# Kernel tuning notes

Measured on AMD Instinct MI355X. Metric: run time of the kernel, lower is better.

## Reference

```python
import jax, jax.numpy as jnp
import numpy as np

B, T, D, F, E, K = 2, 2048, 1024, 4096, 8, 2

def setup_inputs() -> dict:
    key = jax.random.key(0)
    k0, k1, k2, k3 = jax.random.split(key, 4)
    return {
        "x": jax.random.normal(k0, (B, T, D), jnp.float32),
        "Wg": jax.random.normal(k1, (D, E), jnp.float32) * (D ** -0.5),
        "W1": jax.random.normal(k2, (E, D, F), jnp.float32) * (D ** -0.5),
        "b1": jnp.zeros((E, F), jnp.float32),
        "W2": jax.random.normal(k3, (E, F, D), jnp.float32) * (F ** -0.5),
        "b2": jnp.zeros((E, D), jnp.float32),
        "topk": K,
    }

def reference(x, Wg, W1, b1, W2, b2, topk):
    n_experts = Wg.shape[-1]
    # Gating logits [B, T, E]
    gating = jnp.einsum('btd,de->bte', x, Wg)
    _, idx = jax.lax.top_k(gating, topk)
    # 0/1 mask of selected experts per token [B, T, E]
    mask = jax.nn.one_hot(idx, n_experts, dtype=x.dtype).sum(axis=-2)
    # Source does `gating -= 1/mask - 1`: no-op where mask==1, -inf where mask==0
    gate = jax.nn.softmax(jnp.where(mask > 0, gating, -jnp.inf), axis=-1)
    # Dense masked per-expert compute, exactly as the source (expert(x * mask_e))
    xm = x[:, :, None, :] * mask[:, :, :, None]          # [B, T, E, D]
    h = jax.nn.gelu(jnp.einsum('bted,edf->btef', xm, W1) + b1)  # [B, T, E, F]
    out_e = jnp.einsum('btef,efd->bted', h, W2) + b2     # [B, T, E, D]
    # Gate and sum over experts
    return jnp.sum(out_e * gate[..., None], axis=-2)      # [B, T, D]
```

## Files before the change

kernel.cpp:

```cpp
#include <hip/hip_runtime.h>
#include <hip/hip_bf16.h>
#include <math.h>

#define NB 2
#define NT 2048
#define NTOK 4096
#define DD 1024
#define FF 4096
#define NE 8
#define KSEL 2
#define BM 128
#define BN 128
#define BK 64
#define ROWCAP 9216
#define ROWTILES 72
#define KP2 2

typedef __attribute__((ext_vector_type(8))) short short8_t;
typedef __attribute__((ext_vector_type(4))) float f32x4;

__device__ __forceinline__ unsigned short f2bf(float f){
  unsigned u = __float_as_uint(f);
  unsigned r = (u + 0x7fffu + ((u >> 16) & 1u)) >> 16;
  return (unsigned short)r;
}

__device__ __forceinline__ int xcd_swz(int lin, int nwg){
  int q = nwg >> 3, r = nwg & 7;
  int xcd = lin & 7, idx = lin >> 3;
  return (xcd < r ? xcd * (q + 1) : r * (q + 1) + (xcd - r) * q) + idx;
}

#define GLOAD_LDS(g, l) \
  __builtin_amdgcn_global_load_lds((const __attribute__((address_space(1))) void*)(g), \
                                   (__attribute__((address_space(3))) void*)(l), 16, 0, 0)


__global__ void k_prep(const float* __restrict__ x, const float* __restrict__ wg,
                       short* __restrict__ xb, int* __restrict__ topk_idx,
                       float* __restrict__ topk_gate, int* __restrict__ counts){
  int wid = threadIdx.x >> 6, lane = threadIdx.x & 63;
  int t = blockIdx.x * 4 + wid;
  const float* xr = x + (size_t)t * DD;
  short* xbr = xb + (size_t)t * DD;
  double acc[NE];
#pragma unroll
  for (int e = 0; e < NE; ++e) acc[e] = 0.0;
#pragma unroll
  for (int p = 0; p < 4; ++p){
    int d = p * 256 + lane * 4;
    float4 v = *(const float4*)(xr + d);
    short4 o;
    o.x = (short)f2bf(v.x); o.y = (short)f2bf(v.y);
    o.z = (short)f2bf(v.z); o.w = (short)f2bf(v.w);
    *(short4*)(xbr + d) = o;
    const float* w0 = wg + (size_t)d * NE;
    float vv[4] = {v.x, v.y, v.z, v.w};
#pragma unroll
    for (int j = 0; j < 4; ++j){
      double xv = (double)vv[j];
#pragma unroll
      for (int e = 0; e < NE; ++e) acc[e] += xv * (double)w0[j * NE + e];
    }
  }
#pragma unroll
  for (int e = 0; e < NE; ++e){
#pragma unroll
    for (int s = 32; s; s >>= 1) acc[e] += __shfl_xor(acc[e], s, 64);
  }
  if (lane == 0){
    int i0 = 0; double v0 = acc[0];
#pragma unroll
    for (int e = 1; e < NE; ++e) if (acc[e] > v0){ v0 = acc[e]; i0 = e; }
    int i1 = -1; double v1 = -1e300;
#pragma unroll
    for (int e = 0; e < NE; ++e) if (e != i0 && acc[e] > v1){ v1 = acc[e]; i1 = e; }
    double g0 = 1.0 / (1.0 + exp(v1 - v0));
    topk_idx[2 * t] = i0; topk_idx[2 * t + 1] = i1;
    topk_gate[2 * t] = (float)g0; topk_gate[2 * t + 1] = (float)(1.0 - g0);
    atomicAdd(&counts[i0], 1);
    atomicAdd(&counts[i1], 1);
  }
}


__global__ void k_transpose_all(const float* __restrict__ W1, const float* __restrict__ W2,
                                short* __restrict__ w1t, short* __restrict__ w2t){
  __shared__ short T[64][132];
  int id = blockIdx.x;
  bool isW2 = id >= 4096;
  int rem = id & 4095;
  int e = rem >> 9;
  int tr = rem & 511;
  int R, C, c0, r0;
  const float* in; short* out;
  if (!isW2){ R = DD; C = FF; c0 = (tr & 63) * 64; r0 = (tr >> 6) * 128;
              in = W1 + (size_t)e * R * C; out = w1t + (size_t)e * R * C; }
  else      { R = FF; C = DD; c0 = (tr & 15) * 64; r0 = (tr >> 4) * 128;
              in = W2 + (size_t)e * R * C; out = w2t + (size_t)e * R * C; }
  int t = threadIdx.x;
  int rr = t >> 4, c4 = (t & 15) * 4;
#pragma unroll
  for (int p = 0; p < 8; ++p){
    int row = p * 16 + rr;
    float4 v = *(const float4*)(in + (size_t)(r0 + row) * C + c0 + c4);
    T[c4 + 0][row] = (short)f2bf(v.x);
    T[c4 + 1][row] = (short)f2bf(v.y);
    T[c4 + 2][row] = (short)f2bf(v.z);
    T[c4 + 3][row] = (short)f2bf(v.w);
  }
  __syncthreads();
  int c8 = (t & 15) * 8;
#pragma unroll
  for (int q = 0; q < 4; ++q){
    int orow = q * 16 + rr;
    short4 lo = *(const short4*)&T[orow][c8];
    short4 hi = *(const short4*)&T[orow][c8 + 4];
    short8_t w;
    w[0] = lo.x; w[1] = lo.y; w[2] = lo.z; w[3] = lo.w;
    w[4] = hi.x; w[5] = hi.y; w[6] = hi.z; w[7] = hi.w;
    *(short8_t*)(out + (size_t)(c0 + orow) * R + r0 + c8) = w;
  }
}


__global__ void k_route_all(const int* __restrict__ counts, const int* __restrict__ topk_idx,
                            const float* __restrict__ topk_gate, int* __restrict__ poff_g,
                            int* __restrict__ row_token, float* __restrict__ row_gate,
                            int* __restrict__ slot_of){
  __shared__ int poff[NE + 1], cur[NE], rends[NE];
  if (threadIdx.x == 0){
    int off = 0;
    for (int e = 0; e < NE; ++e){
      poff[e] = off; cur[e] = off; rends[e] = off + counts[e];
      off += (counts[e] + BM - 1) & ~(BM - 1);
    }
    poff[NE] = off;
    for (int e = 0; e <= NE; ++e) poff_g[e] = poff[e];
  }
  __syncthreads();
  for (int t = threadIdx.x; t < NTOK; t += 256){
#pragma unroll
    for (int k = 0; k < KSEL; ++k){
      int e = topk_idx[2 * t + k];
      float g = topk_gate[2 * t + k];
      int slot = atomicAdd(&cur[e], 1);
      row_token[slot] = t;
      row_gate[slot] = g;
      slot_of[2 * t + k] = slot;
    }
  }
  __syncthreads();
#pragma unroll
  for (int e = 0; e < NE; ++e)
    for (int s = rends[e] + (int)threadIdx.x; s < poff[e + 1]; s += 256){
      row_token[s] = 0; row_gate[s] = 0.f;
    }
}


__launch_bounds__(256, 4)
__global__ void k_gemm1(const short* __restrict__ xb, const short* __restrict__ w1t,
                        const float* __restrict__ b1, short* __restrict__ h,
                        const int* __restrict__ row_token, const int* __restrict__ poff){
  __shared__ short As[BM * BK];
  __shared__ short Bs[BN * BK];
  int lin = blockIdx.x + ROWTILES * blockIdx.y;
  int wg = xcd_swz(lin, ROWTILES * (FF / BN));
  int bx = wg >> 5, by = wg & 31;
  int row0 = bx * BM;
  if (row0 >= poff[NE]) return;
  int e = 0;
  while (row0 >= poff[e + 1]) ++e;
  int n0 = by * BN;
  int tid = threadIdx.x;

  const short* asrc[4]; const short* bsrc[4];
#pragma unroll
  for (int p = 0; p < 4; ++p){
    int L = p * 256 + tid;
    int r = L >> 3, cs = L & 7;
    int cd = cs ^ (r & 7);
    int tok = row_token[row0 + r];
    asrc[p] = xb + (size_t)tok * DD + cd * 8;
    bsrc[p] = w1t + (size_t)e * FF * DD + (size_t)(n0 + r) * DD + cd * 8;
  }
  short* alds = As + tid * 8;
  short* blds = Bs + tid * 8;

  f32x4 acc[4][4];
#pragma unroll
  for (int i = 0; i < 4; ++i)
#pragma unroll
    for (int j = 0; j < 4; ++j) acc[i][j] = (f32x4){0.f, 0.f, 0.f, 0.f};

  int wid = tid >> 6, lane = tid & 63;
  int wr = wid >> 1, wc = wid & 1;
  int lrow = lane & 15, lk = lane >> 4;

  for (int k0 = 0; k0 < DD; k0 += BK){
#pragma unroll
    for (int p = 0; p < 4; ++p){
      GLOAD_LDS(asrc[p] + k0, alds + p * 2048);
      GLOAD_LDS(bsrc[p] + k0, blds + p * 2048);
    }
    __syncthreads();
#pragma unroll
    for (int kk = 0; kk < 2; ++kk){
      short8_t a[4], b[4];
      int c = kk * 4 + lk;
#pragma unroll
      for (int m = 0; m < 4; ++m){
        int r = wr * 64 + m * 16 + lrow;
        a[m] = *(const short8_t*)(As + r * BK + ((c ^ (r & 7)) * 8));
      }
#pragma unroll
      for (int n = 0; n < 4; ++n){
        int r = wc * 64 + n * 16 + lrow;
        b[n] = *(const short8_t*)(Bs + r * BK + ((c ^ (r & 7)) * 8));
      }
#pragma unroll
      for (int m = 0; m < 4; ++m)
#pragma unroll
        for (int n = 0; n < 4; ++n)
          acc[m][n] = __builtin_amdgcn_mfma_f32_16x16x32_bf16(a[m], b[n], acc[m][n], 0, 0, 0);
    }
    __syncthreads();
  }

  const float* b1e = b1 + (size_t)e * FF;
#pragma unroll
  for (int n = 0; n < 4; ++n){
    int col = n0 + wc * 64 + n * 16 + lrow;
    float bias = b1e[col];
#pragma unroll
    for (int m = 0; m < 4; ++m){
#pragma unroll
      for (int j = 0; j < 4; ++j){
        int row = row0 + wr * 64 + m * 16 + lk * 4 + j;
        float v = acc[m][n][j] + bias;
        float u = 0.7978845608028654f * (v + 0.044715f * v * v * v);
        float g = v / (1.0f + __expf(-2.0f * u));
        h[(size_t)row * FF + col] = (short)f2bf(g);
      }
    }
  }
}


__launch_bounds__(256, 4)
__global__ void k_gemm2(const short* __restrict__ h, const short* __restrict__ w2t,
                        const float* __restrict__ b2, float* __restrict__ ya,
                        float* __restrict__ yb, const int* __restrict__ poff){
  __shared__ short As[BM * BK];
  __shared__ short Bs[BN * BK];
  int lin = blockIdx.x + ROWTILES * (blockIdx.y + (DD / BN) * blockIdx.z);
  int wg = xcd_swz(lin, ROWTILES * (DD / BN) * KP2);
  int by = wg & 7, bx = (wg >> 3) % ROWTILES, kz = (wg >> 3) / ROWTILES;
  int row0 = bx * BM;
  if (row0 >= poff[NE]) return;
  int e = 0;
  while (row0 >= poff[e + 1]) ++e;
  int n0 = by * BN;
  int tid = threadIdx.x;

  const short* asrc[4]; const short* bsrc[4];
#pragma unroll
  for (int p = 0; p < 4; ++p){
    int L = p * 256 + tid;
    int r = L >> 3, cs = L & 7;
    int cd = cs ^ (r & 7);
    asrc[p] = h + (size_t)(row0 + r) * FF + cd * 8;
    bsrc[p] = w2t + (size_t)e * DD * FF + (size_t)(n0 + r) * FF + cd * 8;
  }
  short* alds = As + tid * 8;
  short* blds = Bs + tid * 8;

  f32x4 acc[4][4];
#pragma unroll
  for (int i = 0; i < 4; ++i)
#pragma unroll
    for (int j = 0; j < 4; ++j) acc[i][j] = (f32x4){0.f, 0.f, 0.f, 0.f};

  int wid = tid >> 6, lane = tid & 63;
  int wr = wid >> 1, wc = wid & 1;
  int lrow = lane & 15, lk = lane >> 4;

  int kbeg = kz * (FF / KP2), kend = kbeg + FF / KP2;
  for (int k0 = kbeg; k0 < kend; k0 += BK){
#pragma unroll
    for (int p = 0; p < 4; ++p){
      GLOAD_LDS(asrc[p] + k0, alds + p * 2048);
      GLOAD_LDS(bsrc[p] + k0, blds + p * 2048);
    }
    __syncthreads();
#pragma unroll
    for (int kk = 0; kk < 2; ++kk){
      short8_t a[4], b[4];
      int c = kk * 4 + lk;
#pragma unroll
      for (int m = 0; m < 4; ++m){
        int r = wr * 64 + m * 16 + lrow;
        a[m] = *(const short8_t*)(As + r * BK + ((c ^ (r & 7)) * 8));
      }
#pragma unroll
      for (int n = 0; n < 4; ++n){
        int r = wc * 64 + n * 16 + lrow;
        b[n] = *(const short8_t*)(Bs + r * BK + ((c ^ (r & 7)) * 8));
      }
#pragma unroll
      for (int m = 0; m < 4; ++m)
#pragma unroll
        for (int n = 0; n < 4; ++n)
          acc[m][n] = __builtin_amdgcn_mfma_f32_16x16x32_bf16(a[m], b[n], acc[m][n], 0, 0, 0);
    }
    __syncthreads();
  }

  float* y = (kz == 0) ? ya : yb;
  const float* b2e = b2 + (size_t)e * DD;
#pragma unroll
  for (int n = 0; n < 4; ++n){
    int col = n0 + wc * 64 + n * 16 + lrow;
    float bias = (kz == 0) ? b2e[col] : 0.0f;
#pragma unroll
    for (int m = 0; m < 4; ++m){
#pragma unroll
      for (int j = 0; j < 4; ++j){
        int row = row0 + wr * 64 + m * 16 + lk * 4 + j;
        y[(size_t)row * DD + col] = acc[m][n][j] + bias;
      }
    }
  }
}


__global__ void k_combine(const float* __restrict__ ya, const float* __restrict__ yb,
                          const int* __restrict__ slot_of, const float* __restrict__ topk_gate,
                          float* __restrict__ out){
  int i = blockIdx.x * 256 + threadIdx.x;
  int t = i >> 8;
  int c4 = (i & 255) * 4;
  int s0 = slot_of[2 * t], s1 = slot_of[2 * t + 1];
  float g0 = topk_gate[2 * t], g1 = topk_gate[2 * t + 1];
  float4 a0 = *(const float4*)(ya + (size_t)s0 * DD + c4);
  float4 b0 = *(const float4*)(yb + (size_t)s0 * DD + c4);
  float4 a1 = *(const float4*)(ya + (size_t)s1 * DD + c4);
  float4 b1 = *(const float4*)(yb + (size_t)s1 * DD + c4);
  float4 o;
  o.x = g0 * (a0.x + b0.x) + g1 * (a1.x + b1.x);
  o.y = g0 * (a0.y + b0.y) + g1 * (a1.y + b1.y);
  o.z = g0 * (a0.z + b0.z) + g1 * (a1.z + b1.z);
  o.w = g0 * (a0.w + b0.w) + g1 * (a1.w + b1.w);
  *(float4*)(out + (size_t)t * DD + c4) = o;
}


extern "C" void kernel_launch(void* const* d_in, const int* in_sizes, int n_in,
                              void* d_out, int out_size, void* d_ws, size_t ws_size,
                              hipStream_t stream){
  (void)in_sizes; (void)n_in; (void)out_size; (void)ws_size;
  const float* x  = (const float*)d_in[0];
  const float* Wg = (const float*)d_in[1];
  const float* W1 = (const float*)d_in[2];
  const float* b1 = (const float*)d_in[3];
  const float* W2 = (const float*)d_in[4];
  const float* b2 = (const float*)d_in[5];
  float* out = (float*)d_out;
  char* ws = (char*)d_ws;

  int*   counts    = (int*)(ws + 0);
  int*   poff      = (int*)(ws + 256);
  int*   topk_idx  = (int*)(ws + 1024);
  float* topk_gate = (float*)(ws + 33792);
  int*   row_token = (int*)(ws + 66560);
  float* row_gate  = (float*)(ws + 103424);
  int*   slot_of   = (int*)(ws + 140288);
  short* xb        = (short*)(ws + 173056);
  short* w1t       = (short*)(ws + 8561664);
  short* w2t       = (short*)(ws + 75670528);
  short* h         = (short*)(ws + 142779392);
  float* ya        = (float*)(ws + 173056);
  float* yb        = (float*)(ws + 37921792);

  hipMemsetAsync(counts, 0, 32, stream);

  k_prep<<<dim3(NTOK / 4), 256, 0, stream>>>(x, Wg, xb, topk_idx, topk_gate, counts);
  k_transpose_all<<<dim3(8192), 256, 0, stream>>>(W1, W2, w1t, w2t);
  k_route_all<<<dim3(1), 256, 0, stream>>>(counts, topk_idx, topk_gate, poff,
                                           row_token, row_gate, slot_of);
  k_gemm1<<<dim3(ROWTILES, FF / BN), 256, 0, stream>>>(xb, w1t, b1, h, row_token, poff);
  k_gemm2<<<dim3(ROWTILES, DD / BN, KP2), 256, 0, stream>>>(h, w2t, b2, ya, yb, poff);
  k_combine<<<dim3(NTOK * DD / 4 / 256), 256, 0, stream>>>(ya, yb, slot_of, topk_gate, out);
}
```

Before: 473.9 us.

## Rewrite expert GEMMs with 256x256 double-buffered tiles and atomic gated scatter

Both expert GEMMs move to 512-thread blocks computing 256x256 tiles. The K loop now double-buffers LDS and interleaves the next tile's async global-to-LDS loads with MFMA phases, using raw barriers and priority hints. The combine kernel and the split-K y buffers are replaced by per-element gated atomicAdd into a zeroed output, with split-K raised to 4. GEMM1's epilogue stages GELU results through LDS to make vector stores. The weight transposes are split so W2's transpose runs after GEMM1 and reuses the xb workspace. The change aims for more operand reuse and latency hiding, but the float atomics add contention and make summation order nondeterministic.

```diff
diff --git a/kernel.cpp b/kernel.cpp
--- a/kernel.cpp
+++ b/kernel.cpp
@@ -2,27 +2,22 @@
 #include <hip/hip_bf16.h>
 #include <math.h>
 
-#define NB 2
-#define NT 2048
 #define NTOK 4096
 #define DD 1024
 #define FF 4096
 #define NE 8
 #define KSEL 2
-#define BM 128
-#define BN 128
 #define BK 64
-#define ROWCAP 9216
-#define ROWTILES 72
-#define KP2 2
+#define PADR 256
+#define MT 40
+#define KP2 4
 
 typedef __attribute__((ext_vector_type(8))) short short8_t;
 typedef __attribute__((ext_vector_type(4))) float f32x4;
 
 __device__ __forceinline__ unsigned short f2bf(float f){
   unsigned u = __float_as_uint(f);
-  unsigned r = (u + 0x7fffu + ((u >> 16) & 1u)) >> 16;
-  return (unsigned short)r;
+  return (unsigned short)((u + 0x7fffu + ((u >> 16) & 1u)) >> 16);
 }
 
 __device__ __forceinline__ int xcd_swz(int lin, int nwg){
@@ -34,6 +29,11 @@
 #define GLOAD_LDS(g, l) \
   __builtin_amdgcn_global_load_lds((const __attribute__((address_space(1))) void*)(g), \
                                    (__attribute__((address_space(3))) void*)(l), 16, 0, 0)
+#define VMCNT0 asm volatile("s_waitcnt vmcnt(0)" ::: "memory")
+#define RAWBAR __builtin_amdgcn_s_barrier()
+#define SCHEDB __builtin_amdgcn_sched_barrier(0)
+#define PRIO1 __builtin_amdgcn_s_setprio(1)
+#define PRIO0 __builtin_amdgcn_s_setprio(0)
 
 
 __global__ void k_prep(const float* __restrict__ x, const float* __restrict__ wg,
@@ -84,20 +84,16 @@
 }
 
 
-__global__ void k_transpose_all(const float* __restrict__ W1, const float* __restrict__ W2,
-                                short* __restrict__ w1t, short* __restrict__ w2t){
+__global__ void k_transpose(const float* __restrict__ W, short* __restrict__ Wt, int isW2){
   __shared__ short T[64][132];
   int id = blockIdx.x;
-  bool isW2 = id >= 4096;
-  int rem = id & 4095;
-  int e = rem >> 9;
-  int tr = rem & 511;
+  int e = id >> 9;
+  int tr = id & 511;
   int R, C, c0, r0;
-  const float* in; short* out;
-  if (!isW2){ R = DD; C = FF; c0 = (tr & 63) * 64; r0 = (tr >> 6) * 128;
-              in = W1 + (size_t)e * R * C; out = w1t + (size_t)e * R * C; }
-  else      { R = FF; C = DD; c0 = (tr & 15) * 64; r0 = (tr >> 4) * 128;
-              in = W2 + (size_t)e * R * C; out = w2t + (size_t)e * R * C; }
+  if (!isW2){ R = DD; C = FF; c0 = (tr & 63) * 64; r0 = (tr >> 6) * 128; }
+  else      { R = FF; C = DD; c0 = (tr & 15) * 64; r0 = (tr >> 4) * 128; }
+  const float* in = W + (size_t)e * R * C;
+  short* out = Wt + (size_t)e * R * C;
   int t = threadIdx.x;
   int rr = t >> 4, c4 = (t & 15) * 4;
 #pragma unroll
@@ -126,14 +122,13 @@
 
 __global__ void k_route_all(const int* __restrict__ counts, const int* __restrict__ topk_idx,
                             const float* __restrict__ topk_gate, int* __restrict__ poff_g,
-                            int* __restrict__ row_token, float* __restrict__ row_gate,
-                            int* __restrict__ slot_of){
+                            int* __restrict__ row_token, float* __restrict__ row_gate){
   __shared__ int poff[NE + 1], cur[NE], rends[NE];
   if (threadIdx.x == 0){
     int off = 0;
     for (int e = 0; e < NE; ++e){
       poff[e] = off; cur[e] = off; rends[e] = off + counts[e];
-      off += (counts[e] + BM - 1) & ~(BM - 1);
+      off += (counts[e] + PADR - 1) & ~(PADR - 1);
     }
     poff[NE] = off;
     for (int e = 0; e <= NE; ++e) poff_g[e] = poff[e];
@@ -143,11 +138,9 @@
 #pragma unroll
     for (int k = 0; k < KSEL; ++k){
       int e = topk_idx[2 * t + k];
-      float g = topk_gate[2 * t + k];
       int slot = atomicAdd(&cur[e], 1);
       row_token[slot] = t;
-      row_gate[slot] = g;
-      slot_of[2 * t + k] = slot;
+      row_gate[slot] = topk_gate[2 * t + k];
     }
   }
   __syncthreads();
@@ -159,200 +152,272 @@
 }
 
 
-__launch_bounds__(256, 4)
+__launch_bounds__(512, 2)
 __global__ void k_gemm1(const short* __restrict__ xb, const short* __restrict__ w1t,
                         const float* __restrict__ b1, short* __restrict__ h,
                         const int* __restrict__ row_token, const int* __restrict__ poff){
-  __shared__ short As[BM * BK];
-  __shared__ short Bs[BN * BK];
-  int lin = blockIdx.x + ROWTILES * blockIdx.y;
-  int wg = xcd_swz(lin, ROWTILES * (FF / BN));
-  int bx = wg >> 5, by = wg & 31;
-  int row0 = bx * BM;
+  __shared__ short As[2][2][8192];
+  __shared__ short Bs[2][2][8192];
+  int lin = xcd_swz(blockIdx.x, MT * (FF / 256));
+  int chunk = lin / 80, idx = lin % 80;
+  int bx = chunk * 5 + idx % 5;
+  int by = idx / 5;
+  int row0 = bx * 256;
   if (row0 >= poff[NE]) return;
   int e = 0;
   while (row0 >= poff[e + 1]) ++e;
-  int n0 = by * BN;
+  int n0 = by * 256;
   int tid = threadIdx.x;
-
-  const short* asrc[4]; const short* bsrc[4];
-#pragma unroll
-  for (int p = 0; p < 4; ++p){
-    int L = p * 256 + tid;
-    int r = L >> 3, cs = L & 7;
-    int cd = cs ^ (r & 7);
-    int tok = row_token[row0 + r];
-    asrc[p] = xb + (size_t)tok * DD + cd * 8;
-    bsrc[p] = w1t + (size_t)e * FF * DD + (size_t)(n0 + r) * DD + cd * 8;
-  }
-  short* alds = As + tid * 8;
-  short* blds = Bs + tid * 8;
-
-  f32x4 acc[4][4];
-#pragma unroll
-  for (int i = 0; i < 4; ++i)
-#pragma unroll
-    for (int j = 0; j < 4; ++j) acc[i][j] = (f32x4){0.f, 0.f, 0.f, 0.f};
-
   int wid = tid >> 6, lane = tid & 63;
   int wr = wid >> 1, wc = wid & 1;
   int lrow = lane & 15, lk = lane >> 4;
 
-  for (int k0 = 0; k0 < DD; k0 += BK){
-#pragma unroll
-    for (int p = 0; p < 4; ++p){
-      GLOAD_LDS(asrc[p] + k0, alds + p * 2048);
-      GLOAD_LDS(bsrc[p] + k0, blds + p * 2048);
-    }
-    __syncthreads();
-#pragma unroll
-    for (int kk = 0; kk < 2; ++kk){
-      short8_t a[4], b[4];
-      int c = kk * 4 + lk;
-#pragma unroll
-      for (int m = 0; m < 4; ++m){
-        int r = wr * 64 + m * 16 + lrow;
-        a[m] = *(const short8_t*)(As + r * BK + ((c ^ (r & 7)) * 8));
-      }
-#pragma unroll
-      for (int n = 0; n < 4; ++n){
-        int r = wc * 64 + n * 16 + lrow;
-        b[n] = *(const short8_t*)(Bs + r * BK + ((c ^ (r & 7)) * 8));
-      }
-#pragma unroll
-      for (int m = 0; m < 4; ++m)
-#pragma unroll
-        for (int n = 0; n < 4; ++n)
-          acc[m][n] = __builtin_amdgcn_mfma_f32_16x16x32_bf16(a[m], b[n], acc[m][n], 0, 0, 0);
-    }
-    __syncthreads();
+  const short* a_src[2][2]; const short* b_src[2][2];
+  {
+    int r = tid >> 3, cd = (tid & 7) ^ (r & 7);
+    int r2 = (512 + tid) >> 3, cd2 = ((512 + tid) & 7) ^ (r2 & 7);
+#pragma unroll
+    for (int h2 = 0; h2 < 2; ++h2){
+      int tokA = row_token[row0 + h2 * 128 + r];
+      int tokB = row_token[row0 + h2 * 128 + r2];
+      a_src[h2][0] = xb + (size_t)tokA * DD + cd * 8;
+      a_src[h2][1] = xb + (size_t)tokB * DD + cd2 * 8;
+      b_src[h2][0] = w1t + (size_t)e * FF * DD + (size_t)(n0 + h2 * 128 + r) * DD + cd * 8;
+      b_src[h2][1] = w1t + (size_t)e * FF * DD + (size_t)(n0 + h2 * 128 + r2) * DD + cd2 * 8;
+    }
+  }
+
+  f32x4 acc[4][8];
+#pragma unroll
+  for (int i = 0; i < 4; ++i)
+#pragma unroll
+    for (int j = 0; j < 8; ++j) acc[i][j] = (f32x4){0.f, 0.f, 0.f, 0.f};
+
+  auto SA = [&](int nb, int k0){
+#pragma unroll
+    for (int h2 = 0; h2 < 2; ++h2){
+      GLOAD_LDS(a_src[h2][0] + k0, &As[nb][h2][0] + tid * 8);
+      GLOAD_LDS(a_src[h2][1] + k0, &As[nb][h2][0] + 4096 + tid * 8);
+    }
+  };
+  auto SB = [&](int nb, int k0){
+#pragma unroll
+    for (int h2 = 0; h2 < 2; ++h2){
+      GLOAD_LDS(b_src[h2][0] + k0, &Bs[nb][h2][0] + tid * 8);
+      GLOAD_LDS(b_src[h2][1] + k0, &Bs[nb][h2][0] + 4096 + tid * 8);
+    }
+  };
+  auto rdA = [&](const short* Ab, int kk, short8_t* av){
+#pragma unroll
+    for (int m = 0; m < 4; ++m){
+      int r = (wr & 1) * 64 + m * 16 + lrow;
+      av[m] = *(const short8_t*)(Ab + r * 64 + (((kk * 4 + lk) ^ (r & 7)) << 3));
+    }
+  };
+  auto rdB = [&](const short* Bb, int kk, short8_t* bv){
+#pragma unroll
+    for (int n = 0; n < 4; ++n){
+      int r = wc * 64 + n * 16 + lrow;
+      bv[n] = *(const short8_t*)(Bb + r * 64 + (((kk * 4 + lk) ^ (r & 7)) << 3));
+    }
+  };
+  auto MF = [&](int nh, short8_t* av, short8_t* bv){
+#pragma unroll
+    for (int m = 0; m < 4; ++m)
+#pragma unroll
+      for (int n = 0; n < 4; ++n)
+        acc[m][nh * 4 + n] = __builtin_amdgcn_mfma_f32_16x16x32_bf16(av[m], bv[n], acc[m][nh * 4 + n], 0, 0, 0);
+  };
+
+  SA(0, 0); SB(0, 0);
+  VMCNT0; RAWBAR; SCHEDB;
+
+  const int NKT = DD / BK;
+#pragma unroll 1
+  for (int g = 0; g < NKT; ++g){
+    int b = g & 1, nb = b ^ 1;
+    int k1 = (g + 1) * BK;
+    bool more = (g + 1 < NKT);
+    const short* Ab = &As[b][wr >> 1][0];
+    short8_t av[4], bv[4];
+    if (more) SA(nb, k1);
+    rdA(Ab, 0, av); rdB(&Bs[b][0][0], 0, bv);
+    RAWBAR; SCHEDB; PRIO1; MF(0, av, bv); PRIO0; RAWBAR; SCHEDB;
+    if (more) SB(nb, k1);
+    rdB(&Bs[b][1][0], 0, bv);
+    RAWBAR; SCHEDB; PRIO1; MF(1, av, bv); PRIO0; RAWBAR; SCHEDB;
+    rdA(Ab, 1, av); rdB(&Bs[b][0][0], 1, bv);
+    RAWBAR; SCHEDB; PRIO1; MF(0, av, bv); PRIO0; RAWBAR; SCHEDB;
+    rdB(&Bs[b][1][0], 1, bv);
+    RAWBAR; SCHEDB; PRIO1; MF(1, av, bv); PRIO0;
+    if (more) VMCNT0;
+    RAWBAR; SCHEDB;
   }
 
   const float* b1e = b1 + (size_t)e * FF;
-#pragma unroll
-  for (int n = 0; n < 4; ++n){
-    int col = n0 + wc * 64 + n * 16 + lrow;
-    float bias = b1e[col];
-#pragma unroll
-    for (int m = 0; m < 4; ++m){
-#pragma unroll
-      for (int j = 0; j < 4; ++j){
-        int row = row0 + wr * 64 + m * 16 + lk * 4 + j;
-        float v = acc[m][n][j] + bias;
-        float u = 0.7978845608028654f * (v + 0.044715f * v * v * v);
-        float g = v / (1.0f + __expf(-2.0f * u));
-        h[(size_t)row * FF + col] = (short)f2bf(g);
-      }
-    }
-  }
-}
-
-
-__launch_bounds__(256, 4)
-__global__ void k_gemm2(const short* __restrict__ h, const short* __restrict__ w2t,
-                        const float* __restrict__ b2, float* __restrict__ ya,
-                        float* __restrict__ yb, const int* __restrict__ poff){
-  __shared__ short As[BM * BK];
-  __shared__ short Bs[BN * BK];
-  int lin = blockIdx.x + ROWTILES * (blockIdx.y + (DD / BN) * blockIdx.z);
-  int wg = xcd_swz(lin, ROWTILES * (DD / BN) * KP2);
-  int by = wg & 7, bx = (wg >> 3) % ROWTILES, kz = (wg >> 3) / ROWTILES;
-  int row0 = bx * BM;
+  float bias8[8];
+#pragma unroll
+  for (int nh = 0; nh < 2; ++nh)
+#pragma unroll
+    for (int n = 0; n < 4; ++n)
+      bias8[nh * 4 + n] = b1e[n0 + nh * 128 + wc * 64 + n * 16 + lrow];
+  short* E = &As[0][0][0] + wid * 2048;
+#pragma unroll 1
+  for (int m = 0; m < 4; ++m){
+#pragma unroll
+    for (int nh = 0; nh < 2; ++nh)
+#pragma unroll
+      for (int n = 0; n < 4; ++n)
+#pragma unroll
+        for (int j = 0; j < 4; ++j){
+          float v = acc[m][nh * 4 + n][j] + bias8[nh * 4 + n];
+          float u = 0.7978845608028654f * (v + 0.044715f * v * v * v);
+          float gl = v / (1.0f + __expf(-2.0f * u));
+          E[(lk * 4 + j) * 128 + nh * 64 + n * 16 + lrow] = (short)f2bf(gl);
+        }
+#pragma unroll
+    for (int q = 0; q < 4; ++q){
+      int id = q * 64 + lane;
+      int r = id >> 4;
+      int c8 = id & 15;
+      short8_t w = *(const short8_t*)(E + r * 128 + c8 * 8);
+      int row = row0 + wr * 64 + m * 16 + r;
+      int col = n0 + (c8 >> 3) * 128 + wc * 64 + (c8 & 7) * 8;
+      *(short8_t*)(h + (size_t)row * FF + col) = w;
+    }
+  }
+}
+
+
+__launch_bounds__(512, 2)
+__global__ void k_gemm2(const short* __restrict__ hA, const short* __restrict__ w2t,
+                        const float* __restrict__ b2, float* __restrict__ out,
+                        const int* __restrict__ row_token, const float* __restrict__ row_gate,
+                        const int* __restrict__ poff){
+  __shared__ short As[2][2][8192];
+  __shared__ short Bs[2][2][8192];
+  int lin = xcd_swz(blockIdx.x, MT * (DD / 256) * KP2);
+  int chunk = lin / 80, idx = lin % 80;
+  int bx = chunk * 5 + idx % 5;
+  int by = (idx / 5) & 3;
+  int kz = idx / 20;
+  int row0 = bx * 256;
   if (row0 >= poff[NE]) return;
   int e = 0;
   while (row0 >= poff[e + 1]) ++e;
-  int n0 = by * BN;
+  int n0 = by * 256;
+  int kbeg = kz * (FF / KP2);
   int tid = threadIdx.x;
-
-  const short* asrc[4]; const short* bsrc[4];
-#pragma unroll
-  for (int p = 0; p < 4; ++p){
-    int L = p * 256 + tid;
-    int r = L >> 3, cs = L & 7;
-    int cd = cs ^ (r & 7);
-    asrc[p] = h + (size_t)(row0 + r) * FF + cd * 8;
-    bsrc[p] = w2t + (size_t)e * DD * FF + (size_t)(n0 + r) * FF + cd * 8;
-  }
-  short* alds = As + tid * 8;
-  short* blds = Bs + tid * 8;
-
-  f32x4 acc[4][4];
-#pragma unroll
-  for (int i = 0; i < 4; ++i)
-#pragma unroll
-    for (int j = 0; j < 4; ++j) acc[i][j] = (f32x4){0.f, 0.f, 0.f, 0.f};
-
   int wid = tid >> 6, lane = tid & 63;
   int wr = wid >> 1, wc = wid & 1;
   int lrow = lane & 15, lk = lane >> 4;
 
-  int kbeg = kz * (FF / KP2), kend = kbeg + FF / KP2;
-  for (int k0 = kbeg; k0 < kend; k0 += BK){
-#pragma unroll
-    for (int p = 0; p < 4; ++p){
-      GLOAD_LDS(asrc[p] + k0, alds + p * 2048);
-      GLOAD_LDS(bsrc[p] + k0, blds + p * 2048);
-    }
-    __syncthreads();
-#pragma unroll
-    for (int kk = 0; kk < 2; ++kk){
-      short8_t a[4], b[4];
-      int c = kk * 4 + lk;
-#pragma unroll
-      for (int m = 0; m < 4; ++m){
-        int r = wr * 64 + m * 16 + lrow;
-        a[m] = *(const short8_t*)(As + r * BK + ((c ^ (r & 7)) * 8));
+  const short* a_src[2][2]; const short* b_src[2][2];
+  {
+    int r = tid >> 3, cd = (tid & 7) ^ (r & 7);
+    int r2 = (512 + tid) >> 3, cd2 = ((512 + tid) & 7) ^ (r2 & 7);
+#pragma unroll
+    for (int h2 = 0; h2 < 2; ++h2){
+      a_src[h2][0] = hA + (size_t)(row0 + h2 * 128 + r) * FF + kbeg + cd * 8;
+      a_src[h2][1] = hA + (size_t)(row0 + h2 * 128 + r2) * FF + kbeg + cd2 * 8;
+      b_src[h2][0] = w2t + (size_t)e * DD * FF + (size_t)(n0 + h2 * 128 + r) * FF + kbeg + cd * 8;
+      b_src[h2][1] = w2t + (size_t)e * DD * FF + (size_t)(n0 + h2 * 128 + r2) * FF + kbeg + cd2 * 8;
+    }
+  }
+
+  f32x4 acc[4][8];
+#pragma unroll
+  for (int i = 0; i < 4; ++i)
+#pragma unroll
+    for (int j = 0; j < 8; ++j) acc[i][j] = (f32x4){0.f, 0.f, 0.f, 0.f};
+
+  auto SA = [&](int nb, int k0){
+#pragma unroll
+    for (int h2 = 0; h2 < 2; ++h2){
+      GLOAD_LDS(a_src[h2][0] + k0, &As[nb][h2][0] + tid * 8);
+      GLOAD_LDS(a_src[h2][1] + k0, &As[nb][h2][0] + 4096 + tid * 8);
+    }
+  };
+  auto SB = [&](int nb, int k0){
+#pragma unroll
+    for (int h2 = 0; h2 < 2; ++h2){
+      GLOAD_LDS(b_src[h2][0] + k0, &Bs[nb][h2][0] + tid * 8);
+      GLOAD_LDS(b_src[h2][1] + k0, &Bs[nb][h2][0] + 4096 + tid * 8);
+    }
+  };
+  auto rdA = [&](const short* Ab, int kk, short8_t* av){
+#pragma unroll
+    for (int m = 0; m < 4; ++m){
+      int r = (wr & 1) * 64 + m * 16 + lrow;
+      av[m] = *(const short8_t*)(Ab + r * 64 + (((kk * 4 + lk) ^ (r & 7)) << 3));
+    }
+  };
+  auto rdB = [&](const short* Bb, int kk, short8_t* bv){
+#pragma unroll
+    for (int n = 0; n < 4; ++n){
+      int r = wc * 64 + n * 16 + lrow;
+      bv[n] = *(const short8_t*)(Bb + r * 64 + (((kk * 4 + lk) ^ (r & 7)) << 3));
+    }
+  };
+  auto MF = [&](int nh, short8_t* av, short8_t* bv){
+#pragma unroll
+    for (int m = 0; m < 4; ++m)
+#pragma unroll
+      for (int n = 0; n < 4; ++n)
+        acc[m][nh * 4 + n] = __builtin_amdgcn_mfma_f32_16x16x32_bf16(av[m], bv[n], acc[m][nh * 4 + n], 0, 0, 0);
+  };
+
+  SA(0, 0); SB(0, 0);
+  VMCNT0; RAWBAR; SCHEDB;
+
+  const int NKT = (FF / KP2) / BK;
+#pragma unroll 1
+  for (int g = 0; g < NKT; ++g){
+    int b = g & 1, nb = b ^ 1;
+    int k1 = (g + 1) * BK;
+    bool more = (g + 1 < NKT);
+    const short* Ab = &As[b][wr >> 1][0];
+    short8_t av[4], bv[4];
+    if (more) SA(nb, k1);
+    rdA(Ab, 0, av); rdB(&Bs[b][0][0], 0, bv);
+    RAWBAR; SCHEDB; PRIO1; MF(0, av, bv); PRIO0; RAWBAR; SCHEDB;
+    if (more) SB(nb, k1);
+    rdB(&Bs[b][1][0], 0, bv);
+    RAWBAR; SCHEDB; PRIO1; MF(1, av, bv); PRIO0; RAWBAR; SCHEDB;
+    rdA(Ab, 1, av); rdB(&Bs[b][0][0], 1, bv);
+    RAWBAR; SCHEDB; PRIO1; MF(0, av, bv); PRIO0; RAWBAR; SCHEDB;
+    rdB(&Bs[b][1][0], 1, bv);
+    RAWBAR; SCHEDB; PRIO1; MF(1, av, bv); PRIO0;
+    if (more) VMCNT0;
+    RAWBAR; SCHEDB;
+  }
+
+  const float* b2e = b2 + (size_t)e * DD;
+  float bias8[8];
+#pragma unroll
+  for (int nh = 0; nh < 2; ++nh)
+#pragma unroll
+    for (int n = 0; n < 4; ++n)
+      bias8[nh * 4 + n] = (kz == 0) ? b2e[n0 + nh * 128 + wc * 64 + n * 16 + lrow] : 0.0f;
+#pragma unroll
+  for (int m = 0; m < 4; ++m){
+#pragma unroll
+    for (int j = 0; j < 4; ++j){
+      int row = row0 + wr * 64 + m * 16 + lk * 4 + j;
+      float gt = row_gate[row];
+      if (gt != 0.f){
+        int tok = row_token[row];
+        float* orow = out + (size_t)tok * DD;
+#pragma unroll
+        for (int nh = 0; nh < 2; ++nh)
+#pragma unroll
+          for (int n = 0; n < 4; ++n){
+            int col = n0 + nh * 128 + wc * 64 + n * 16 + lrow;
+            atomicAdd(&orow[col], gt * (acc[m][nh * 4 + n][j] + bias8[nh * 4 + n]));
+          }
       }
-#pragma unroll
-      for (int n = 0; n < 4; ++n){
-        int r = wc * 64 + n * 16 + lrow;
-        b[n] = *(const short8_t*)(Bs + r * BK + ((c ^ (r & 7)) * 8));
-      }
-#pragma unroll
-      for (int m = 0; m < 4; ++m)
-#pragma unroll
-        for (int n = 0; n < 4; ++n)
-          acc[m][n] = __builtin_amdgcn_mfma_f32_16x16x32_bf16(a[m], b[n], acc[m][n], 0, 0, 0);
-    }
-    __syncthreads();
-  }
-
-  float* y = (kz == 0) ? ya : yb;
-  const float* b2e = b2 + (size_t)e * DD;
-#pragma unroll
-  for (int n = 0; n < 4; ++n){
-    int col = n0 + wc * 64 + n * 16 + lrow;
-    float bias = (kz == 0) ? b2e[col] : 0.0f;
-#pragma unroll
-    for (int m = 0; m < 4; ++m){
-#pragma unroll
-      for (int j = 0; j < 4; ++j){
-        int row = row0 + wr * 64 + m * 16 + lk * 4 + j;
-        y[(size_t)row * DD + col] = acc[m][n][j] + bias;
-      }
-    }
-  }
-}
-
-
-__global__ void k_combine(const float* __restrict__ ya, const float* __restrict__ yb,
-                          const int* __restrict__ slot_of, const float* __restrict__ topk_gate,
-                          float* __restrict__ out){
-  int i = blockIdx.x * 256 + threadIdx.x;
-  int t = i >> 8;
-  int c4 = (i & 255) * 4;
-  int s0 = slot_of[2 * t], s1 = slot_of[2 * t + 1];
-  float g0 = topk_gate[2 * t], g1 = topk_gate[2 * t + 1];
-  float4 a0 = *(const float4*)(ya + (size_t)s0 * DD + c4);
-  float4 b0 = *(const float4*)(yb + (size_t)s0 * DD + c4);
-  float4 a1 = *(const float4*)(ya + (size_t)s1 * DD + c4);
-  float4 b1 = *(const float4*)(yb + (size_t)s1 * DD + c4);
-  float4 o;
-  o.x = g0 * (a0.x + b0.x) + g1 * (a1.x + b1.x);
-  o.y = g0 * (a0.y + b0.y) + g1 * (a1.y + b1.y);
-  o.z = g0 * (a0.z + b0.z) + g1 * (a1.z + b1.z);
-  o.w = g0 * (a0.w + b0.w) + g1 * (a1.w + b1.w);
-  *(float4*)(out + (size_t)t * DD + c4) = o;
+    }
+  }
 }
 
 
@@ -370,26 +435,25 @@
   char* ws = (char*)d_ws;
 
   int*   counts    = (int*)(ws + 0);
-  int*   poff      = (int*)(ws + 256);
+  int*   poff      = (int*)(ws + 64);
   int*   topk_idx  = (int*)(ws + 1024);
   float* topk_gate = (float*)(ws + 33792);
   int*   row_token = (int*)(ws + 66560);
-  float* row_gate  = (float*)(ws + 103424);
-  int*   slot_of   = (int*)(ws + 140288);
-  short* xb        = (short*)(ws + 173056);
-  short* w1t       = (short*)(ws + 8561664);
-  short* w2t       = (short*)(ws + 75670528);
-  short* h         = (short*)(ws + 142779392);
-  float* ya        = (float*)(ws + 173056);
-  float* yb        = (float*)(ws + 37921792);
-
-  hipMemsetAsync(counts, 0, 32, stream);
+  float* row_gate  = (float*)(ws + 107520);
+  short* xb        = (short*)(ws + 148480);
+  short* w1t       = (short*)(ws + 8537088);
+  short* h         = (short*)(ws + 75645952);
+  short* w2t       = (short*)(ws + 148480);
+
+  hipMemsetAsync(counts, 0, 64, stream);
+  hipMemsetAsync(out, 0, (size_t)NTOK * DD * sizeof(float), stream);
 
   k_prep<<<dim3(NTOK / 4), 256, 0, stream>>>(x, Wg, xb, topk_idx, topk_gate, counts);
-  k_transpose_all<<<dim3(8192), 256, 0, stream>>>(W1, W2, w1t, w2t);
+  k_transpose<<<dim3(4096), 256, 0, stream>>>(W1, w1t, 0);
   k_route_all<<<dim3(1), 256, 0, stream>>>(counts, topk_idx, topk_gate, poff,
-                                           row_token, row_gate, slot_of);
-  k_gemm1<<<dim3(ROWTILES, FF / BN), 256, 0, stream>>>(xb, w1t, b1, h, row_token, poff);
-  k_gemm2<<<dim3(ROWTILES, DD / BN, KP2), 256, 0, stream>>>(h, w2t, b2, ya, yb, poff);
-  k_combine<<<dim3(NTOK * DD / 4 / 256), 256, 0, stream>>>(ya, yb, slot_of, topk_gate, out);
-}
+                                           row_token, row_gate);
+  k_gemm1<<<dim3(MT * (FF / 256)), 512, 0, stream>>>(xb, w1t, b1, h, row_token, poff);
+  k_transpose<<<dim3(4096), 256, 0, stream>>>(W2, w2t, 1);
+  k_gemm2<<<dim3(MT * (DD / 256) * KP2), 512, 0, stream>>>(h, w2t, b2, out,
+                                                           row_token, row_gate, poff);
+}
```

Measured after the change: 624.1 us. 1.32x slower.
